# Optimization experiments

Hardware: AMD Instinct MI355X
Metric: run time of the kernel (lower is better)

## Reference

```python
import jax, jax.numpy as jnp
import numpy as np

N = 100000
E = 3200000
IN = 128
HID = 128   # 2 * out_channels
OUT = 64


def setup_inputs() -> dict:
    key = jax.random.key(0)
    ks = jax.random.split(key, 8)
    x = jax.random.normal(ks[0], (N, IN), dtype=jnp.float32)
    edge_index = jax.random.randint(ks[1], (2, E), 0, N, dtype=jnp.int64)
    s1 = 1.0 / np.sqrt(IN)
    s2 = 1.0 / np.sqrt(HID)
    # PyG GraphConv per layer: lin_rel (with bias) applied to aggregated neighbors,
    # lin_root (no bias) applied to the node itself. Linear weight is (out, in).
    W1_rel = jax.random.uniform(ks[2], (HID, IN), jnp.float32, -s1, s1)
    b1 = jax.random.uniform(ks[3], (HID,), jnp.float32, -s1, s1)
    W1_root = jax.random.uniform(ks[4], (HID, IN), jnp.float32, -s1, s1)
    W2_rel = jax.random.uniform(ks[5], (OUT, HID), jnp.float32, -s2, s2)
    b2 = jax.random.uniform(ks[6], (OUT,), jnp.float32, -s2, s2)
    W2_root = jax.random.uniform(ks[7], (OUT, HID), jnp.float32, -s2, s2)
    return {"x": x, "edge_index": edge_index, "W1_rel": W1_rel, "b1": b1,
            "W1_root": W1_root, "W2_rel": W2_rel, "b2": b2, "W2_root": W2_root}


def _graph_conv(h, src, dst, W_rel, b, W_root, num_nodes):
    # sum-aggregate neighbor features at dst, then affine combine with root term
    agg = jax.ops.segment_sum(h[src], dst, num_segments=num_nodes)  # [N, d_in]
    return agg @ W_rel.T + b + h @ W_root.T


def reference(x, edge_index, W1_rel, b1, W1_root, W2_rel, b2, W2_root):
    src = edge_index[0]
    dst = edge_index[1]
    n = x.shape[0]
    h = _graph_conv(x, src, dst, W1_rel, b1, W1_root, n)
    h = jax.nn.relu(h)  # dropout p=0.0 -> identity
    return _graph_conv(h, src, dst, W2_rel, b2, W2_root, n)
```

## Files before the change

kernel.cpp:

```cpp
#include <hip/hip_runtime.h>
#include <hip/hip_bf16.h>


#define EB 8192
#define NB_MAX 512
#define BCAP 12288

typedef __attribute__((ext_vector_type(8))) short bf16x8;
typedef __attribute__((ext_vector_type(4))) float f32x4;
typedef __attribute__((ext_vector_type(2))) float f32x2;

__device__ __forceinline__ uint pack_bf16x2(float a, float b) {
    __hip_bfloat162 p = __float22bfloat162_rn(make_float2(a, b));
    return *(uint*)&p;
}

__device__ __forceinline__ uchar pack_fp8(float v) {
    uint p = __builtin_amdgcn_cvt_pk_fp8_f32(v, v, 0, false);
    return (uchar)(p & 0xff);
}

__device__ __forceinline__ float bflo(uint g) { return __uint_as_float(g << 16); }
__device__ __forceinline__ float bfhi(uint g) { return __uint_as_float(g & 0xffff0000u); }

__device__ __forceinline__ ushort bf16u(float v) {
    __hip_bfloat16 hb = __float2bfloat16(v);
    return *(ushort*)&hb;
}


__global__ __launch_bounds__(256) void bucket_scatter2(const int* __restrict__ src,
                                                       const int* __restrict__ dst, int E,
                                                       int NB, int* __restrict__ bcnt,
                                                       uint* __restrict__ ebuf) {
    __shared__ int hloc[NB_MAX];
    __shared__ int cur[NB_MAX];
    int t = threadIdx.x, blk = blockIdx.x;
    for (int i = t; i < NB; i += 256) hloc[i] = 0;
    __syncthreads();
    int e0 = blk * EB, e1 = min(E, e0 + EB);
    for (int e = e0 + t; e < e1; e += 256) atomicAdd(&hloc[dst[e] >> 8], 1);
    __syncthreads();
    for (int i = t; i < NB; i += 256) {
        int c = hloc[i];
        cur[i] = (c > 0) ? atomicAdd(&bcnt[i], c) : 0;
    }
    __syncthreads();
    for (int e = e0 + t; e < e1; e += 256) {
        int d = dst[e];
        int b = d >> 8;
        int p = atomicAdd(&cur[b], 1);
        if (p < BCAP)
            ebuf[(size_t)b * BCAP + p] = ((uint)(d & 255) << 24) | (uint)src[e];
    }
}

__global__ __launch_bounds__(512) void scan_bases(const int* __restrict__ bcnt, int NB,
                                                  int* __restrict__ bbase) {
    __shared__ int s[512];
    int t = threadIdx.x;
    int v = (t < NB) ? bcnt[t] : 0;
    s[t] = v;
    __syncthreads();
    for (int off = 1; off < 512; off <<= 1) {
        int u = (t >= off) ? s[t - off] : 0;
        __syncthreads();
        s[t] += u;
        __syncthreads();
    }
    if (t < NB) bbase[t] = s[t] - v;
}

__global__ __launch_bounds__(256) void build_csr2(const uint* __restrict__ ebuf,
                                                  const int* __restrict__ bcnt,
                                                  const int* __restrict__ bbase,
                                                  int NB, int N, int E,
                                                  int* __restrict__ rowptr,
                                                  int* __restrict__ col) {
    __shared__ int cnt[256];
    __shared__ int s[256];
    __shared__ int cur[256];
    int b = blockIdx.x, t = threadIdx.x;
    int n_e = min(bcnt[b], BCAP);
    int gbase = bbase[b];
    const uint* eb = ebuf + (size_t)b * BCAP;
    cnt[t] = 0;
    __syncthreads();
    for (int e = t; e < n_e; e += 256) atomicAdd(&cnt[eb[e] >> 24], 1);
    __syncthreads();
    int v = cnt[t];
    s[t] = v;
    __syncthreads();
    for (int off = 1; off < 256; off <<= 1) {
        int u = (t >= off) ? s[t - off] : 0;
        __syncthreads();
        s[t] += u;
        __syncthreads();
    }
    int start = gbase + s[t] - v;
    int node = (b << 8) + t;
    if (node < N) rowptr[node] = start;
    if (b == NB - 1 && t == 0) rowptr[N] = E;
    cur[t] = start;
    __syncthreads();
    for (int e = t; e < n_e; e += 256) {
        uint ev = eb[e];
        int p = atomicAdd(&cur[ev >> 24], 1);
        col[p] = (int)(ev & 0xFFFFFFu);
    }
}


__global__ __launch_bounds__(256) void prep_w(const float* __restrict__ W1_rel,
                                              const float* __restrict__ W1_root,
                                              const float* __restrict__ W2_rel,
                                              const float* __restrict__ W2_root,
                                              ushort* __restrict__ Wb1,
                                              ushort* __restrict__ Wb2) {
    int t = blockIdx.x * 256 + threadIdx.x;
    if (t < 8192) {
        int idx = t * 4;
        int row = idx >> 7, c = idx & 127;
        const float* src = (row < 128) ? W1_rel + (size_t)row * 128 + c
                                       : W1_root + (size_t)(row - 128) * 128 + c;
        float4 v = *(const float4*)src;
        uint2 u;
        u.x = pack_bf16x2(v.x, v.y);
        u.y = pack_bf16x2(v.z, v.w);
        *(uint2*)(Wb1 + idx) = u;
    } else if (t < 12288) {
        int idx = (t - 8192) * 4;
        int row = idx >> 7, c = idx & 127;
        const float* src = (row < 64) ? W2_rel + (size_t)row * 128 + c
                                      : W2_root + (size_t)(row - 64) * 128 + c;
        float4 v = *(const float4*)src;
        uint2 u;
        u.x = pack_bf16x2(v.x, v.y);
        u.y = pack_bf16x2(v.z, v.w);
        *(uint2*)(Wb2 + idx) = u;
    }
}


template <int C, bool A_BF16, bool Y_FP8>
__global__ __launch_bounds__(256, 3) void gemm_direct(const void* __restrict__ Aptr,
                                                      const ushort* __restrict__ Wb16,
                                                      const float* __restrict__ bias,
                                                      void* __restrict__ Yout,
                                                      ushort* __restrict__ Z, int n_rows) {
    const int t = threadIdx.x;
    const int lane = t & 63;
    const int wave = t >> 6;
    const int wm = wave >> 1, wn = wave & 1;
    const int row0 = blockIdx.x * 128;
    const int tn = blockIdx.y;
    const int fr = lane & 15;
    const int quad = lane >> 4;

    f32x4 acc[4][4];
#pragma unroll
    for (int i = 0; i < 4; i++)
#pragma unroll
        for (int j = 0; j < 4; j++) acc[i][j] = (f32x4){0.f, 0.f, 0.f, 0.f};

    int ar[4];
#pragma unroll
    for (int mt = 0; mt < 4; ++mt) {
        int r = row0 + wm * 64 + mt * 16 + fr;
        ar[mt] = (r < n_rows) ? r : (n_rows - 1);
    }
    const int brbase = tn * 128 + wn * 64;

#pragma unroll
    for (int kk = 0; kk < 4; ++kk) {
        const int kb = kk * 32 + quad * 8;
        bf16x8 a[4], b[4];
#pragma unroll
        for (int mt = 0; mt < 4; ++mt) {
            if (A_BF16) {
                a[mt] = *(const bf16x8*)((const ushort*)Aptr + (size_t)ar[mt] * 128 + kb);
            } else {
                const float* p = (const float*)Aptr + (size_t)ar[mt] * 128 + kb;
                float4 v0 = *(const float4*)p;
                float4 v1 = *(const float4*)(p + 4);
                uint4 u;
                u.x = pack_bf16x2(v0.x, v0.y);
                u.y = pack_bf16x2(v0.z, v0.w);
                u.z = pack_bf16x2(v1.x, v1.y);
                u.w = pack_bf16x2(v1.z, v1.w);
                a[mt] = *(bf16x8*)&u;
            }
        }
#pragma unroll
        for (int nt = 0; nt < 4; ++nt)
            b[nt] = *(const bf16x8*)(Wb16 + (size_t)(brbase + nt * 16 + fr) * 128 + kb);
#pragma unroll
        for (int mt = 0; mt < 4; ++mt)
#pragma unroll
            for (int nt = 0; nt < 4; ++nt)
                acc[mt][nt] = __builtin_amdgcn_mfma_f32_16x16x32_bf16(
                    a[mt], b[nt], acc[mt][nt], 0, 0, 0);
    }

#pragma unroll
    for (int nt = 0; nt < 4; ++nt) {
        int gcol = tn * 128 + wn * 64 + nt * 16 + fr;
        if (gcol < C) {
#pragma unroll
            for (int mt = 0; mt < 4; ++mt) {
#pragma unroll
                for (int r = 0; r < 4; ++r) {
                    int grow = row0 + wm * 64 + mt * 16 + quad * 4 + r;
                    if (grow < n_rows) {
                        if (Y_FP8) {
                            ((uchar*)Yout)[(size_t)grow * C + gcol] =
                                pack_fp8(acc[mt][nt][r]);
                        } else {
                            ((ushort*)Yout)[(size_t)grow * C + gcol] =
                                bf16u(acc[mt][nt][r]);
                        }
                    }
                }
            }
        } else {
            float bv = bias[gcol - C];
#pragma unroll
            for (int mt = 0; mt < 4; ++mt) {
#pragma unroll
                for (int r = 0; r < 4; ++r) {
                    int grow = row0 + wm * 64 + mt * 16 + quad * 4 + r;
                    if (grow < n_rows)
                        Z[(size_t)grow * C + (gcol - C)] = bf16u(acc[mt][nt][r] + bv);
                }
            }
        }
    }
}


__global__ __launch_bounds__(256) void agg_relu_l1(const uchar* __restrict__ Y1,
                                                   const ushort* __restrict__ Z1,
                                                   const int* __restrict__ rowptr,
                                                   const int* __restrict__ col,
                                                   ushort* __restrict__ h, int n_nodes) {
    int node = (blockIdx.x * 256 + threadIdx.x) >> 6;
    if (node >= n_nodes) return;
    int lane = threadIdx.x & 63;
    int sub = lane >> 3;
    int cg  = lane & 7;
    int beg = rowptr[node], end = rowptr[node + 1];
    float acc[16];
#pragma unroll
    for (int i = 0; i < 16; i++) acc[i] = 0.f;

    int e = beg;
    for (; e + 16 <= end; e += 16) {
        int s0 = col[e + sub];
        int s1 = col[e + 8 + sub];
        uint4 v0 = *(const uint4*)(Y1 + (size_t)s0 * 128 + cg * 16);
        uint4 v1 = *(const uint4*)(Y1 + (size_t)s1 * 128 + cg * 16);
        f32x2 p;
        p = __builtin_amdgcn_cvt_pk_f32_fp8(v0.x, false); acc[0] += p[0]; acc[1] += p[1];
        p = __builtin_amdgcn_cvt_pk_f32_fp8(v0.x, true);  acc[2] += p[0]; acc[3] += p[1];
        p = __builtin_amdgcn_cvt_pk_f32_fp8(v0.y, false); acc[4] += p[0]; acc[5] += p[1];
        p = __builtin_amdgcn_cvt_pk_f32_fp8(v0.y, true);  acc[6] += p[0]; acc[7] += p[1];
        p = __builtin_amdgcn_cvt_pk_f32_fp8(v0.z, false); acc[8] += p[0]; acc[9] += p[1];
        p = __builtin_amdgcn_cvt_pk_f32_fp8(v0.z, true);  acc[10] += p[0]; acc[11] += p[1];
        p = __builtin_amdgcn_cvt_pk_f32_fp8(v0.w, false); acc[12] += p[0]; acc[13] += p[1];
        p = __builtin_amdgcn_cvt_pk_f32_fp8(v0.w, true);  acc[14] += p[0]; acc[15] += p[1];
        p = __builtin_amdgcn_cvt_pk_f32_fp8(v1.x, false); acc[0] += p[0]; acc[1] += p[1];
        p = __builtin_amdgcn_cvt_pk_f32_fp8(v1.x, true);  acc[2] += p[0]; acc[3] += p[1];
        p = __builtin_amdgcn_cvt_pk_f32_fp8(v1.y, false); acc[4] += p[0]; acc[5] += p[1];
        p = __builtin_amdgcn_cvt_pk_f32_fp8(v1.y, true);  acc[6] += p[0]; acc[7] += p[1];
        p = __builtin_amdgcn_cvt_pk_f32_fp8(v1.z, false); acc[8] += p[0]; acc[9] += p[1];
        p = __builtin_amdgcn_cvt_pk_f32_fp8(v1.z, true);  acc[10] += p[0]; acc[11] += p[1];
        p = __builtin_amdgcn_cvt_pk_f32_fp8(v1.w, false); acc[12] += p[0]; acc[13] += p[1];
        p = __builtin_amdgcn_cvt_pk_f32_fp8(v1.w, true);  acc[14] += p[0]; acc[15] += p[1];
    }
    for (; e < end; e += 8) {
        int ee = e + sub;
        uint4 v = make_uint4(0u, 0u, 0u, 0u);
        if (ee < end)
            v = *(const uint4*)(Y1 + (size_t)col[ee] * 128 + cg * 16);
        f32x2 p;
        p = __builtin_amdgcn_cvt_pk_f32_fp8(v.x, false); acc[0] += p[0]; acc[1] += p[1];
        p = __builtin_amdgcn_cvt_pk_f32_fp8(v.x, true);  acc[2] += p[0]; acc[3] += p[1];
        p = __builtin_amdgcn_cvt_pk_f32_fp8(v.y, false); acc[4] += p[0]; acc[5] += p[1];
        p = __builtin_amdgcn_cvt_pk_f32_fp8(v.y, true);  acc[6] += p[0]; acc[7] += p[1];
        p = __builtin_amdgcn_cvt_pk_f32_fp8(v.z, false); acc[8] += p[0]; acc[9] += p[1];
        p = __builtin_amdgcn_cvt_pk_f32_fp8(v.z, true);  acc[10] += p[0]; acc[11] += p[1];
        p = __builtin_amdgcn_cvt_pk_f32_fp8(v.w, false); acc[12] += p[0]; acc[13] += p[1];
        p = __builtin_amdgcn_cvt_pk_f32_fp8(v.w, true);  acc[14] += p[0]; acc[15] += p[1];
    }

#pragma unroll
    for (int off = 8; off < 64; off <<= 1)
#pragma unroll
        for (int i = 0; i < 16; i++) acc[i] += __shfl_xor(acc[i], off, 64);

    if (sub == 0) {
        const uint4* zp = (const uint4*)(Z1 + (size_t)node * 128 + cg * 16);
        uint4 za = zp[0], zb = zp[1];
        float z[16] = {bflo(za.x), bfhi(za.x), bflo(za.y), bfhi(za.y),
                       bflo(za.z), bfhi(za.z), bflo(za.w), bfhi(za.w),
                       bflo(zb.x), bfhi(zb.x), bflo(zb.y), bfhi(zb.y),
                       bflo(zb.z), bfhi(zb.z), bflo(zb.w), bfhi(zb.w)};
        uint o[8];
#pragma unroll
        for (int q = 0; q < 8; ++q) {
            float r0 = acc[q * 2 + 0] + z[q * 2 + 0];
            float r1 = acc[q * 2 + 1] + z[q * 2 + 1];
            r0 = r0 > 0.f ? r0 : 0.f;
            r1 = r1 > 0.f ? r1 : 0.f;
            o[q] = pack_bf16x2(r0, r1);
        }
        uint* hp = (uint*)(h + (size_t)node * 128) + cg * 8;
        *(uint4*)(hp + 0) = make_uint4(o[0], o[1], o[2], o[3]);
        *(uint4*)(hp + 4) = make_uint4(o[4], o[5], o[6], o[7]);
    }
}


__global__ __launch_bounds__(256) void agg_l2(const ushort* __restrict__ Y2,
                                              const ushort* __restrict__ Z2,
                                              const int* __restrict__ rowptr,
                                              const int* __restrict__ col,
                                              float* __restrict__ out, int n_nodes) {
    int node = (blockIdx.x * 256 + threadIdx.x) >> 6;
    if (node >= n_nodes) return;
    int lane = threadIdx.x & 63;
    int sub = lane >> 3;
    int cg  = lane & 7;
    int beg = rowptr[node], end = rowptr[node + 1];
    float acc[8];
#pragma unroll
    for (int i = 0; i < 8; i++) acc[i] = 0.f;

    int e = beg;
    for (; e + 16 <= end; e += 16) {
        int s0 = col[e + sub];
        int s1 = col[e + 8 + sub];
        uint4 v0 = *(const uint4*)(Y2 + (size_t)s0 * 64 + cg * 8);
        uint4 v1 = *(const uint4*)(Y2 + (size_t)s1 * 64 + cg * 8);
        acc[0] += bflo(v0.x) + bflo(v1.x);
        acc[1] += bfhi(v0.x) + bfhi(v1.x);
        acc[2] += bflo(v0.y) + bflo(v1.y);
        acc[3] += bfhi(v0.y) + bfhi(v1.y);
        acc[4] += bflo(v0.z) + bflo(v1.z);
        acc[5] += bfhi(v0.z) + bfhi(v1.z);
        acc[6] += bflo(v0.w) + bflo(v1.w);
        acc[7] += bfhi(v0.w) + bfhi(v1.w);
    }
    for (; e < end; e += 8) {
        int ee = e + sub;
        uint4 v = make_uint4(0u, 0u, 0u, 0u);
        if (ee < end)
            v = *(const uint4*)(Y2 + (size_t)col[ee] * 64 + cg * 8);
        acc[0] += bflo(v.x);
        acc[1] += bfhi(v.x);
        acc[2] += bflo(v.y);
        acc[3] += bfhi(v.y);
        acc[4] += bflo(v.z);
        acc[5] += bfhi(v.z);
        acc[6] += bflo(v.w);
        acc[7] += bfhi(v.w);
    }

#pragma unroll
    for (int off = 8; off < 64; off <<= 1)
#pragma unroll
        for (int i = 0; i < 8; i++) acc[i] += __shfl_xor(acc[i], off, 64);

    if (sub == 0) {
        uint4 z = *(const uint4*)(Z2 + (size_t)node * 64 + cg * 8);
        float4 o0 = {acc[0] + bflo(z.x), acc[1] + bfhi(z.x),
                     acc[2] + bflo(z.y), acc[3] + bfhi(z.y)};
        float4 o1 = {acc[4] + bflo(z.z), acc[5] + bfhi(z.z),
                     acc[6] + bflo(z.w), acc[7] + bfhi(z.w)};
        float4* op = (float4*)(out + (size_t)node * 64 + cg * 8);
        op[0] = o0;
        op[1] = o1;
    }
}


extern "C" void kernel_launch(void* const* d_in, const int* in_sizes, int n_in,
                              void* d_out, int out_size, void* d_ws, size_t ws_size,
                              hipStream_t stream) {
    const float* x       = (const float*)d_in[0];
    const int*   ei      = (const int*)d_in[1];
    const float* W1_rel  = (const float*)d_in[2];
    const float* b1      = (const float*)d_in[3];
    const float* W1_root = (const float*)d_in[4];
    const float* W2_rel  = (const float*)d_in[5];
    const float* b2      = (const float*)d_in[6];
    const float* W2_root = (const float*)d_in[7];
    float* out = (float*)d_out;

    const int N = in_sizes[0] / 128;
    const int E = in_sizes[1] / 2;
    const int* srcA = ei;
    const int* dstA = ei + E;
    const int NB   = (N + 255) >> 8;
    const int NBLK = (E + EB - 1) / EB;

    char* ws = (char*)d_ws;
    size_t cur = 0;
    auto alloc = [&](size_t bytes) -> void* {
        size_t o = cur;
        cur = (cur + bytes + 511) & ~(size_t)511;
        return (void*)(ws + o);
    };
    uchar*  Y1  = (uchar*)alloc((size_t)N * 128);
    ushort* Z1  = (ushort*)alloc((size_t)N * 128 * 2);
    ushort* h   = (ushort*)alloc((size_t)N * 128 * 2);
    ushort* Y2  = (ushort*)alloc((size_t)N * 64 * 2);
    ushort* Z2  = (ushort*)alloc((size_t)N * 64 * 2);
    int* rowptr = (int*)alloc((size_t)(N + 1) * 4);
    int* colA   = (int*)alloc((size_t)E * 4);
    int* bcnt   = (int*)alloc((size_t)NB_MAX * 4);
    int* bbase  = (int*)alloc((size_t)NB_MAX * 4);
    ushort* Wb1 = (ushort*)alloc((size_t)256 * 128 * 2);
    ushort* Wb2 = (ushort*)alloc((size_t)128 * 128 * 2);
    uint* ebuf  = (uint*)alloc((size_t)NB * BCAP * 4);

    hipMemsetAsync(bcnt, 0, (size_t)NB * 4, stream);
    prep_w<<<48, 256, 0, stream>>>(W1_rel, W1_root, W2_rel, W2_root, Wb1, Wb2);

    bucket_scatter2<<<NBLK, 256, 0, stream>>>(srcA, dstA, E, NB, bcnt, ebuf);
    scan_bases<<<1, 512, 0, stream>>>(bcnt, NB, bbase);
    build_csr2<<<NB, 256, 0, stream>>>(ebuf, bcnt, bbase, NB, N, E, rowptr, colA);

    const int gblk = (N + 127) / 128;
    gemm_direct<128, false, true><<<dim3(gblk, 2), 256, 0, stream>>>(
        x, Wb1, b1, Y1, Z1, N);
    agg_relu_l1<<<(N + 3) / 4, 256, 0, stream>>>(Y1, Z1, rowptr, colA, h, N);
    gemm_direct<64, true, false><<<dim3(gblk, 1), 256, 0, stream>>>(
        h, Wb2, b2, Y2, Z2, N);
    agg_l2<<<(N + 3) / 4, 256, 0, stream>>>(Y2, Z2, rowptr, colA, out, N);
}
```

Baseline: 408.0 us.

## Replace bucketed CSR build with global degree histogram, scan, and atomic scatter

```diff
diff --git a/kernel.cpp b/kernel.cpp
--- a/kernel.cpp
+++ b/kernel.cpp
@@ -2,9 +2,7 @@
 #include <hip/hip_bf16.h>
 
 
-#define EB 8192
-#define NB_MAX 512
-#define BCAP 12288
+#define SCAN_ELEMS 2048
 
 typedef __attribute__((ext_vector_type(8))) short bf16x8;
 typedef __attribute__((ext_vector_type(4))) float f32x4;
@@ -29,66 +27,49 @@
 }
 
 
-__global__ __launch_bounds__(256) void bucket_scatter2(const int* __restrict__ src,
-                                                       const int* __restrict__ dst, int E,
-                                                       int NB, int* __restrict__ bcnt,
-                                                       uint* __restrict__ ebuf) {
-    __shared__ int hloc[NB_MAX];
-    __shared__ int cur[NB_MAX];
-    int t = threadIdx.x, blk = blockIdx.x;
-    for (int i = t; i < NB; i += 256) hloc[i] = 0;
+__global__ __launch_bounds__(256) void deg_hist(const int* __restrict__ dst, int E,
+                                                int* __restrict__ deg) {
+    int i = blockIdx.x * 256 + threadIdx.x;
+    int stride = gridDim.x * 256;
+    for (int e = i; e < E; e += stride) atomicAdd(&deg[dst[e]], 1);
+}
+
+__global__ __launch_bounds__(256) void scan_local(const int* __restrict__ deg, int N,
+                                                  int* __restrict__ rp_local,
+                                                  int* __restrict__ bsum) {
+    __shared__ int s[256];
+    int b = blockIdx.x, t = threadIdx.x;
+    int base = b * SCAN_ELEMS + t * 8;
+    int v[8];
+    int sum = 0;
+#pragma unroll
+    for (int j = 0; j < 8; ++j) {
+        int idx = base + j;
+        v[j] = (idx < N) ? deg[idx] : 0;
+        sum += v[j];
+    }
+    s[t] = sum;
     __syncthreads();
-    int e0 = blk * EB, e1 = min(E, e0 + EB);
-    for (int e = e0 + t; e < e1; e += 256) atomicAdd(&hloc[dst[e] >> 8], 1);
-    __syncthreads();
-    for (int i = t; i < NB; i += 256) {
-        int c = hloc[i];
-        cur[i] = (c > 0) ? atomicAdd(&bcnt[i], c) : 0;
-    }
-    __syncthreads();
-    for (int e = e0 + t; e < e1; e += 256) {
-        int d = dst[e];
-        int b = d >> 8;
-        int p = atomicAdd(&cur[b], 1);
-        if (p < BCAP)
-            ebuf[(size_t)b * BCAP + p] = ((uint)(d & 255) << 24) | (uint)src[e];
-    }
-}
-
-__global__ __launch_bounds__(512) void scan_bases(const int* __restrict__ bcnt, int NB,
-                                                  int* __restrict__ bbase) {
-    __shared__ int s[512];
-    int t = threadIdx.x;
-    int v = (t < NB) ? bcnt[t] : 0;
-    s[t] = v;
-    __syncthreads();
-    for (int off = 1; off < 512; off <<= 1) {
+    for (int off = 1; off < 256; off <<= 1) {
         int u = (t >= off) ? s[t - off] : 0;
         __syncthreads();
         s[t] += u;
         __syncthreads();
     }
-    if (t < NB) bbase[t] = s[t] - v;
-}
-
-__global__ __launch_bounds__(256) void build_csr2(const uint* __restrict__ ebuf,
-                                                  const int* __restrict__ bcnt,
-                                                  const int* __restrict__ bbase,
-                                                  int NB, int N, int E,
-                                                  int* __restrict__ rowptr,
-                                                  int* __restrict__ col) {
-    __shared__ int cnt[256];
+    int run = s[t] - sum;
+#pragma unroll
+    for (int j = 0; j < 8; ++j) {
+        int idx = base + j;
+        if (idx < N) rp_local[idx] = run;
+        run += v[j];
+    }
+    if (t == 255) bsum[b] = s[255];
+}
+
+__global__ __launch_bounds__(256) void scan_bsum(int* __restrict__ bsum, int nb) {
     __shared__ int s[256];
-    __shared__ int cur[256];
-    int b = blockIdx.x, t = threadIdx.x;
-    int n_e = min(bcnt[b], BCAP);
-    int gbase = bbase[b];
-    const uint* eb = ebuf + (size_t)b * BCAP;
-    cnt[t] = 0;
-    __syncthreads();
-    for (int e = t; e < n_e; e += 256) atomicAdd(&cnt[eb[e] >> 24], 1);
-    __syncthreads();
-    int v = cnt[t];
+    int t = threadIdx.x;
+    int v = (t < nb) ? bsum[t] : 0;
     s[t] = v;
     __syncthreads();
     for (int off = 1; off < 256; off <<= 1) {
@@ -97,16 +78,31 @@
         s[t] += u;
         __syncthreads();
     }
-    int start = gbase + s[t] - v;
-    int node = (b << 8) + t;
-    if (node < N) rowptr[node] = start;
-    if (b == NB - 1 && t == 0) rowptr[N] = E;
-    cur[t] = start;
-    __syncthreads();
-    for (int e = t; e < n_e; e += 256) {
-        uint ev = eb[e];
-        int p = atomicAdd(&cur[ev >> 24], 1);
-        col[p] = (int)(ev & 0xFFFFFFu);
+    if (t < nb) bsum[t] = s[t] - v;
+}
+
+__global__ __launch_bounds__(256) void fixup_rowptr(int* __restrict__ rowptr,
+                                                    const int* __restrict__ bsum,
+                                                    int N, int E,
+                                                    int* __restrict__ curptr) {
+    int i = blockIdx.x * 256 + threadIdx.x;
+    int stride = gridDim.x * 256;
+    for (; i <= N; i += stride) {
+        int v = (i < N) ? (rowptr[i] + bsum[i / SCAN_ELEMS]) : E;
+        rowptr[i] = v;
+        if (i < N) curptr[i] = v;
+    }
+}
+
+__global__ __launch_bounds__(256) void scatter_col(const int* __restrict__ src,
+                                                   const int* __restrict__ dst, int E,
+                                                   int* __restrict__ curptr,
+                                                   int* __restrict__ col) {
+    int i = blockIdx.x * 256 + threadIdx.x;
+    int stride = gridDim.x * 256;
+    for (int e = i; e < E; e += stride) {
+        int p = atomicAdd(&curptr[dst[e]], 1);
+        col[p] = src[e];
     }
 }
 
@@ -401,8 +397,7 @@
     const int E = in_sizes[1] / 2;
     const int* srcA = ei;
     const int* dstA = ei + E;
-    const int NB   = (N + 255) >> 8;
-    const int NBLK = (E + EB - 1) / EB;
+    const int NSB = (N + SCAN_ELEMS - 1) / SCAN_ELEMS;
 
     char* ws = (char*)d_ws;
     size_t cur = 0;
@@ -417,19 +412,21 @@
     ushort* Y2  = (ushort*)alloc((size_t)N * 64 * 2);
     ushort* Z2  = (ushort*)alloc((size_t)N * 64 * 2);
     int* rowptr = (int*)alloc((size_t)(N + 1) * 4);
+    int* curptr = (int*)alloc((size_t)N * 4);
     int* colA   = (int*)alloc((size_t)E * 4);
-    int* bcnt   = (int*)alloc((size_t)NB_MAX * 4);
-    int* bbase  = (int*)alloc((size_t)NB_MAX * 4);
+    int* deg    = (int*)alloc((size_t)N * 4);
+    int* bsum   = (int*)alloc((size_t)256 * 4);
     ushort* Wb1 = (ushort*)alloc((size_t)256 * 128 * 2);
     ushort* Wb2 = (ushort*)alloc((size_t)128 * 128 * 2);
-    uint* ebuf  = (uint*)alloc((size_t)NB * BCAP * 4);
-
-    hipMemsetAsync(bcnt, 0, (size_t)NB * 4, stream);
+
+    hipMemsetAsync(deg, 0, (size_t)N * 4, stream);
     prep_w<<<48, 256, 0, stream>>>(W1_rel, W1_root, W2_rel, W2_root, Wb1, Wb2);
 
-    bucket_scatter2<<<NBLK, 256, 0, stream>>>(srcA, dstA, E, NB, bcnt, ebuf);
-    scan_bases<<<1, 512, 0, stream>>>(bcnt, NB, bbase);
-    build_csr2<<<NB, 256, 0, stream>>>(ebuf, bcnt, bbase, NB, N, E, rowptr, colA);
+    deg_hist<<<2048, 256, 0, stream>>>(dstA, E, deg);
+    scan_local<<<NSB, 256, 0, stream>>>(deg, N, rowptr, bsum);
+    scan_bsum<<<1, 256, 0, stream>>>(bsum, NSB);
+    fixup_rowptr<<<128, 256, 0, stream>>>(rowptr, bsum, N, E, curptr);
+    scatter_col<<<2048, 256, 0, stream>>>(srcA, dstA, E, curptr, colA);
 
     const int gblk = (N + 127) / 128;
     gemm_direct<128, false, true><<<dim3(gblk, 2), 256, 0, stream>>>(
```

After: 720.3 us. 76.5% more time.
